# Kernel optimization log

Measured on AMD Instinct MI355X. Metric: run time of the kernel, lower is better.

Reference implementation:

```python
import jax, jax.numpy as jnp
import numpy as np

N = 50000      # nodes
E = 640000     # edges
F_IN = 128     # dataset.num_features
DIM = 128      # mParams['dim']
NC = 6         # dataset.num_classes
BN_EPS = 1e-5


def _bn_eval(z, g, b, rm, rv):
    return g * (z - rm) * jax.lax.rsqrt(rv + BN_EPS) + b


def _gin_layer(h, src, dst, W1, b1, g, be, rm, rv, W2, b2):
    # GINConv (eps=0): nn(x + sum_{j->i} x_j); messages from src aggregated at dst
    agg = jax.ops.segment_sum(h[src], dst, num_segments=N)
    z = (h + agg) @ W1 + b1
    z = jax.nn.relu(_bn_eval(z, g, be, rm, rv))
    z = jax.nn.relu(z @ W2 + b2)
    return z


def setup_inputs() -> dict:
    key = jax.random.key(0)
    ks = jax.random.split(key, 10)
    s = 1.0 / np.sqrt(DIM)
    inp = {
        'x': jax.random.normal(ks[0], (N, F_IN), jnp.float32),
        'edge_index': jax.random.randint(ks[1], (2, E), 0, N, dtype=jnp.int32),
        'batch': jnp.zeros((N,), jnp.int32),
        # conv1 MLP: Linear(F_IN,DIM) -> BN(DIM) -> ReLU -> Linear(DIM,DIM) -> ReLU
        'c1_W1': jax.random.normal(ks[2], (F_IN, DIM), jnp.float32) * s,
        'c1_b1': jnp.zeros((DIM,), jnp.float32),
        'c1_g': jnp.ones((DIM,), jnp.float32),
        'c1_beta': jnp.zeros((DIM,), jnp.float32),
        'c1_rm': jnp.zeros((DIM,), jnp.float32),
        'c1_rv': jnp.ones((DIM,), jnp.float32),
        'c1_W2': jax.random.normal(ks[3], (DIM, DIM), jnp.float32) * s,
        'c1_b2': jnp.zeros((DIM,), jnp.float32),
        # 2 extra GINConv layers (c_depth-1), stacked on leading axis
        'conv_W1': jax.random.normal(ks[4], (2, DIM, DIM), jnp.float32) * s,
        'conv_b1': jnp.zeros((2, DIM), jnp.float32),
        'conv_g': jnp.ones((2, DIM), jnp.float32),
        'conv_beta': jnp.zeros((2, DIM), jnp.float32),
        'conv_rm': jnp.zeros((2, DIM), jnp.float32),
        'conv_rv': jnp.ones((2, DIM), jnp.float32),
        'conv_W2': jax.random.normal(ks[5], (2, DIM, DIM), jnp.float32) * s,
        'conv_b2': jnp.zeros((2, DIM), jnp.float32),
        # 2 linear layers (l_depth)
        'lin_W': jax.random.normal(ks[6], (2, DIM, DIM), jnp.float32) * s,
        'lin_b': jnp.zeros((2, DIM), jnp.float32),
        # classifier Linear(2*DIM, NC)
        'cls_W': jax.random.normal(ks[7], (2 * DIM, NC), jnp.float32) * s,
        'cls_b': jnp.zeros((NC,), jnp.float32),
    }
    return inp


def reference(x, edge_index, batch,
              c1_W1, c1_b1, c1_g, c1_beta, c1_rm, c1_rv, c1_W2, c1_b2,
              conv_W1, conv_b1, conv_g, conv_beta, conv_rm, conv_rv, conv_W2, conv_b2,
              lin_W, lin_b, cls_W, cls_b):
    src, dst = edge_index[0], edge_index[1]
    h = _gin_layer(x, src, dst, c1_W1, c1_b1, c1_g, c1_beta, c1_rm, c1_rv, c1_W2, c1_b2)
    h = jax.nn.relu(h)  # extra .relu() after conv1 (idempotent)
    for i in range(conv_W1.shape[0]):
        h = _gin_layer(h, src, dst, conv_W1[i], conv_b1[i], conv_g[i], conv_beta[i],
                       conv_rm[i], conv_rv[i], conv_W2[i], conv_b2[i])
        h = jax.nn.relu(h)
    for i in range(lin_W.shape[0]):
        h = jax.nn.relu(h @ lin_W[i] + lin_b[i])
    # dropout: eval mode -> identity
    e = jnp.concatenate([h[src], h[dst]], axis=1)  # [E, 2*DIM]
    out = e @ cls_W + cls_b                         # [E, NC]
    return (out, e)
```

## Files before the change

### kernel.cpp

```cpp
#include <hip/hip_runtime.h>
#include <cstddef>
#include <cstdint>

#define NN 50000
#define EE 640000
#define FD 128

typedef float fvec4 __attribute__((ext_vector_type(4)));


__global__ __launch_bounds__(256) void k_zero(int* __restrict__ p) {
  int i = blockIdx.x * 256 + threadIdx.x;
  if (i < NN) p[i] = 0;
}

__global__ __launch_bounds__(256) void k_hist(const int* __restrict__ dst,
                                              int* __restrict__ deg) {
  int e = blockIdx.x * 256 + threadIdx.x;
  atomicAdd(&deg[dst[e]], 1);
}

__global__ __launch_bounds__(1024) void k_scan(const int* __restrict__ deg,
                                               int* __restrict__ off,
                                               int* __restrict__ cur) {
  __shared__ int wsum[16], woff[16];
  __shared__ int carryS;
  const int t = threadIdx.x, lane = t & 63, w = t >> 6;
  if (t == 0) carryS = 0;
  __syncthreads();
  for (int base = 0; base < NN; base += 4096) {
    int i = base + (t << 2);
    int4 dv = make_int4(0, 0, 0, 0);
    if (i < NN) dv = *reinterpret_cast<const int4*>(deg + i);
    int tsum = dv.x + dv.y + dv.z + dv.w;
    int incl = tsum;
#pragma unroll
    for (int d = 1; d < 64; d <<= 1) {
      int u = __shfl_up(incl, d, 64);
      if (lane >= d) incl += u;
    }
    if (lane == 63) wsum[w] = incl;
    __syncthreads();
    if (t == 0) {
      int run = 0;
#pragma unroll
      for (int k = 0; k < 16; ++k) { woff[k] = run; run += wsum[k]; }
    }
    __syncthreads();
    int ebase = (incl - tsum) + woff[w] + carryS;
    if (i < NN) {
      int4 ov;
      ov.x = ebase;
      ov.y = ebase + dv.x;
      ov.z = ov.y + dv.y;
      ov.w = ov.z + dv.z;
      *reinterpret_cast<int4*>(off + i) = ov;
      *reinterpret_cast<int4*>(cur + i) = ov;
    }
    __syncthreads();
    if (t == 0) carryS += woff[15] + wsum[15];
    __syncthreads();
  }
}

__global__ __launch_bounds__(256) void k_fill(const int* __restrict__ src,
                                              const int* __restrict__ dst,
                                              int* __restrict__ cur,
                                              int* __restrict__ ssrc) {
  int e = blockIdx.x * 256 + threadIdx.x;
  int d = dst[e];
  int pos = atomicAdd(&cur[d], 1);
  ssrc[pos] = src[e];
}

__global__ __launch_bounds__(256) void k_agg(const float* __restrict__ h,
                                             const int* __restrict__ off,
                                             const int* __restrict__ deg,
                                             const int* __restrict__ ssrc,
                                             float* __restrict__ agg) {
  int node = blockIdx.x * 8 + (threadIdx.x >> 5);
  int lane = threadIdx.x & 31;
  int f = lane << 2;
  float4 acc = *reinterpret_cast<const float4*>(h + (size_t)node * FD + f);
  int n = deg[node];
  const int* sl = ssrc + off[node];
  int j = 0;
  for (; j + 8 <= n; j += 8) {
    int s0 = sl[j], s1 = sl[j + 1], s2 = sl[j + 2], s3 = sl[j + 3];
    int s4 = sl[j + 4], s5 = sl[j + 5], s6 = sl[j + 6], s7 = sl[j + 7];
    float4 v0 = *reinterpret_cast<const float4*>(h + (size_t)s0 * FD + f);
    float4 v1 = *reinterpret_cast<const float4*>(h + (size_t)s1 * FD + f);
    float4 v2 = *reinterpret_cast<const float4*>(h + (size_t)s2 * FD + f);
    float4 v3 = *reinterpret_cast<const float4*>(h + (size_t)s3 * FD + f);
    float4 v4 = *reinterpret_cast<const float4*>(h + (size_t)s4 * FD + f);
    float4 v5 = *reinterpret_cast<const float4*>(h + (size_t)s5 * FD + f);
    float4 v6 = *reinterpret_cast<const float4*>(h + (size_t)s6 * FD + f);
    float4 v7 = *reinterpret_cast<const float4*>(h + (size_t)s7 * FD + f);
    float tx0 = (v0.x + v1.x) + (v2.x + v3.x);
    float ty0 = (v0.y + v1.y) + (v2.y + v3.y);
    float tz0 = (v0.z + v1.z) + (v2.z + v3.z);
    float tw0 = (v0.w + v1.w) + (v2.w + v3.w);
    float tx1 = (v4.x + v5.x) + (v6.x + v7.x);
    float ty1 = (v4.y + v5.y) + (v6.y + v7.y);
    float tz1 = (v4.z + v5.z) + (v6.z + v7.z);
    float tw1 = (v4.w + v5.w) + (v6.w + v7.w);
    acc.x += tx0 + tx1; acc.y += ty0 + ty1; acc.z += tz0 + tz1; acc.w += tw0 + tw1;
  }
  for (; j + 4 <= n; j += 4) {
    int s0 = sl[j], s1 = sl[j + 1], s2 = sl[j + 2], s3 = sl[j + 3];
    float4 v0 = *reinterpret_cast<const float4*>(h + (size_t)s0 * FD + f);
    float4 v1 = *reinterpret_cast<const float4*>(h + (size_t)s1 * FD + f);
    float4 v2 = *reinterpret_cast<const float4*>(h + (size_t)s2 * FD + f);
    float4 v3 = *reinterpret_cast<const float4*>(h + (size_t)s3 * FD + f);
    acc.x += (v0.x + v1.x) + (v2.x + v3.x);
    acc.y += (v0.y + v1.y) + (v2.y + v3.y);
    acc.z += (v0.z + v1.z) + (v2.z + v3.z);
    acc.w += (v0.w + v1.w) + (v2.w + v3.w);
  }
  for (; j < n; ++j) {
    int s = sl[j];
    float4 v = *reinterpret_cast<const float4*>(h + (size_t)s * FD + f);
    acc.x += v.x; acc.y += v.y; acc.z += v.z; acc.w += v.w;
  }
  *reinterpret_cast<float4*>(agg + (size_t)node * FD + f) = acc;
}

__global__ __launch_bounds__(256) void k_gemm(const float* __restrict__ A,
                                              const float* __restrict__ W,
                                              const float* __restrict__ bias,
                                              const float* __restrict__ gg,
                                              const float* __restrict__ bb,
                                              const float* __restrict__ rm,
                                              const float* __restrict__ rv,
                                              int use_bn,
                                              float* __restrict__ O, int M) {
  __shared__ float At[32][132];
  __shared__ float Ws[32][132];
  const int t  = threadIdx.x;
  const int tx = t & 15;
  const int ty = t >> 4;
  const int rowBase = blockIdx.x * 128;

  float acc[8][8] = {};

  for (int kc = 0; kc < 4; ++kc) {
    const int k0 = kc << 5;
#pragma unroll
    for (int i = 0; i < 4; ++i) {
      int fl = t + (i << 8);
      int row = fl & 127;
      int kg  = (fl >> 7) << 2;
      int r = rowBase + row;
      float4 v = make_float4(0.f, 0.f, 0.f, 0.f);
      if (r < M) v = *reinterpret_cast<const float4*>(A + (size_t)r * FD + k0 + kg);
      At[kg + 0][row] = v.x;
      At[kg + 1][row] = v.y;
      At[kg + 2][row] = v.z;
      At[kg + 3][row] = v.w;
    }
#pragma unroll
    for (int i = 0; i < 4; ++i) {
      int fl = t + (i << 8);
      int wr = fl >> 5;
      int wc = (fl & 31) << 2;
      *reinterpret_cast<float4*>(&Ws[wr][wc]) =
          *reinterpret_cast<const float4*>(W + (size_t)(k0 + wr) * FD + wc);
    }
    __syncthreads();

#pragma unroll 8
    for (int k = 0; k < 32; ++k) {
      const float4 a0 = *reinterpret_cast<const float4*>(&At[k][ty << 3]);
      const float4 a1 = *reinterpret_cast<const float4*>(&At[k][(ty << 3) + 4]);
      const float4 w0 = *reinterpret_cast<const float4*>(&Ws[k][tx << 2]);
      const float4 w1 = *reinterpret_cast<const float4*>(&Ws[k][64 + (tx << 2)]);
      const float av[8] = {a0.x, a0.y, a0.z, a0.w, a1.x, a1.y, a1.z, a1.w};
      const float wv[8] = {w0.x, w0.y, w0.z, w0.w, w1.x, w1.y, w1.z, w1.w};
#pragma unroll
      for (int i2 = 0; i2 < 8; ++i2)
#pragma unroll
        for (int j = 0; j < 8; ++j)
          acc[i2][j] = fmaf(av[i2], wv[j], acc[i2][j]);
    }
    __syncthreads();
  }

  float sc[8], sh[8];
#pragma unroll
  for (int j = 0; j < 8; ++j) {
    int c = (j < 4) ? ((tx << 2) + j) : (64 + (tx << 2) + (j - 4));
    if (use_bn) {
      float s = gg[c] * rsqrtf(rv[c] + 1e-5f);
      sc[j] = s;
      sh[j] = (bias[c] - rm[c]) * s + bb[c];
    } else {
      sc[j] = 1.f;
      sh[j] = bias[c];
    }
  }
#pragma unroll
  for (int i = 0; i < 8; ++i) {
    int r = rowBase + (ty << 3) + i;
    if (r < M) {
      float o[8];
#pragma unroll
      for (int j = 0; j < 8; ++j) {
        float v = fmaf(acc[i][j], sc[j], sh[j]);
        o[j] = v > 0.f ? v : 0.f;
      }
      *reinterpret_cast<float4*>(O + (size_t)r * FD + (tx << 2)) =
          make_float4(o[0], o[1], o[2], o[3]);
      *reinterpret_cast<float4*>(O + (size_t)r * FD + 64 + (tx << 2)) =
          make_float4(o[4], o[5], o[6], o[7]);
    }
  }
}

__global__ __launch_bounds__(256) void k_uv(const float* __restrict__ h,
                                            const float* __restrict__ clsW,
                                            float* __restrict__ U,
                                            float* __restrict__ V) {
  int node = blockIdx.x * 8 + (threadIdx.x >> 5);
  int lane = threadIdx.x & 31;
  int f = lane << 2;
  float4 v = *reinterpret_cast<const float4*>(h + (size_t)node * FD + f);
  float p[12];
#pragma unroll
  for (int c = 0; c < 6; ++c) {
    p[c] = fmaf(v.x, clsW[(size_t)(f + 0) * 6 + c],
           fmaf(v.y, clsW[(size_t)(f + 1) * 6 + c],
           fmaf(v.z, clsW[(size_t)(f + 2) * 6 + c],
                v.w * clsW[(size_t)(f + 3) * 6 + c])));
    p[6 + c] = fmaf(v.x, clsW[(size_t)(FD + f + 0) * 6 + c],
               fmaf(v.y, clsW[(size_t)(FD + f + 1) * 6 + c],
               fmaf(v.z, clsW[(size_t)(FD + f + 2) * 6 + c],
                    v.w * clsW[(size_t)(FD + f + 3) * 6 + c])));
  }
#pragma unroll
  for (int m = 16; m >= 1; m >>= 1) {
#pragma unroll
    for (int c = 0; c < 12; ++c) p[c] += __shfl_xor(p[c], m, 64);
  }
  float outv = 0.f;
#pragma unroll
  for (int c = 0; c < 12; ++c) outv = (lane == c) ? p[c] : outv;
  if (lane < 6)       U[(size_t)node * 6 + lane] = outv;
  else if (lane < 12) V[(size_t)node * 6 + (lane - 6)] = outv;
}

__global__ __launch_bounds__(256) void k_edge(const float* __restrict__ h,
                                              const int* __restrict__ src,
                                              const int* __restrict__ dst,
                                              const float* __restrict__ U,
                                              const float* __restrict__ V,
                                              const float* __restrict__ clsB,
                                              float* __restrict__ outL,
                                              float* __restrict__ outE) {
  int eid  = blockIdx.x * 4 + (threadIdx.x >> 6);
  int lane = threadIdx.x & 63;
  int s = src[eid];
  int d = dst[eid];
  int node = (lane < 32) ? s : d;
  int f = (lane & 31) << 2;
  fvec4 v = *reinterpret_cast<const fvec4*>(h + (size_t)node * FD + f);
  __builtin_nontemporal_store(v, reinterpret_cast<fvec4*>(outE + (size_t)eid * 256 + (lane << 2)));
  if (lane < 6) {
    float lv = U[(size_t)s * 6 + lane] + V[(size_t)d * 6 + lane] + clsB[lane];
    __builtin_nontemporal_store(lv, outL + (size_t)eid * 6 + lane);
  }
}

extern "C" void kernel_launch(void* const* d_in, const int* in_sizes, int n_in,
                              void* d_out, int out_size, void* d_ws, size_t ws_size,
                              hipStream_t stream) {
  const float* x     = (const float*)d_in[0];
  const int*   ei    = (const int*)d_in[1];
  const int*   src   = ei;
  const int*   dst   = ei + EE;
  const float* c1_W1 = (const float*)d_in[3];
  const float* c1_b1 = (const float*)d_in[4];
  const float* c1_g  = (const float*)d_in[5];
  const float* c1_be = (const float*)d_in[6];
  const float* c1_rm = (const float*)d_in[7];
  const float* c1_rv = (const float*)d_in[8];
  const float* c1_W2 = (const float*)d_in[9];
  const float* c1_b2 = (const float*)d_in[10];
  const float* cv_W1 = (const float*)d_in[11];
  const float* cv_b1 = (const float*)d_in[12];
  const float* cv_g  = (const float*)d_in[13];
  const float* cv_be = (const float*)d_in[14];
  const float* cv_rm = (const float*)d_in[15];
  const float* cv_rv = (const float*)d_in[16];
  const float* cv_W2 = (const float*)d_in[17];
  const float* cv_b2 = (const float*)d_in[18];
  const float* ln_W  = (const float*)d_in[19];
  const float* ln_b  = (const float*)d_in[20];
  const float* clsW  = (const float*)d_in[21];
  const float* clsB  = (const float*)d_in[22];

  float* buf0 = (float*)d_ws;
  float* buf1 = buf0 + (size_t)NN * FD;
  float* Uu   = buf1 + (size_t)NN * FD;
  float* Vv   = Uu + (size_t)NN * 6;

  float* outL = (float*)d_out;
  float* outE = outL + (size_t)EE * 6;

  const size_t outFloats = (size_t)EE * 262;
  const size_t scrInts   = (size_t)NN * 3 + (size_t)EE;
  const size_t scrStart  = (outFloats - scrInts) & ~(size_t)3;
  int* deg  = (int*)d_out + scrStart;
  int* off  = deg + NN;
  int* curp = off + NN;
  int* ssrc = curp + NN;

  dim3 B(256);
  const int gZero   = (NN + 255) / 256;
  const int gEdgeWk = EE / 256;
  const int gAgg    = NN / 8;
  const int gGemm   = (NN + 127) / 128;
  const int gUV     = NN / 8;
  const int gEdge   = EE / 4;

  k_zero<<<gZero, B, 0, stream>>>(deg);
  k_hist<<<gEdgeWk, B, 0, stream>>>(dst, deg);
  k_scan<<<1, dim3(1024), 0, stream>>>(deg, off, curp);
  k_fill<<<gEdgeWk, B, 0, stream>>>(src, dst, curp, ssrc);

  float* bufs[2] = {buf0, buf1};

  k_agg<<<gAgg, B, 0, stream>>>(x, off, deg, ssrc, buf0);
  k_gemm<<<gGemm, B, 0, stream>>>(buf0, c1_W1, c1_b1, c1_g, c1_be, c1_rm, c1_rv, 1, buf1, NN);
  k_gemm<<<gGemm, B, 0, stream>>>(buf1, c1_W2, c1_b2, nullptr, nullptr, nullptr, nullptr, 0, buf0, NN);
  int pp = 0;

  for (int l = 0; l < 2; ++l) {
    float* hc = bufs[pp];
    float* ho = bufs[1 - pp];
    k_agg<<<gAgg, B, 0, stream>>>(hc, off, deg, ssrc, ho);
    k_gemm<<<gGemm, B, 0, stream>>>(ho, cv_W1 + (size_t)l * FD * FD, cv_b1 + l * FD,
                                    cv_g + l * FD, cv_be + l * FD, cv_rm + l * FD,
                                    cv_rv + l * FD, 1, hc, NN);
    k_gemm<<<gGemm, B, 0, stream>>>(hc, cv_W2 + (size_t)l * FD * FD, cv_b2 + l * FD,
                                    nullptr, nullptr, nullptr, nullptr, 0, ho, NN);
    pp = 1 - pp;
  }

  for (int l = 0; l < 2; ++l) {
    k_gemm<<<gGemm, B, 0, stream>>>(bufs[pp], ln_W + (size_t)l * FD * FD, ln_b + l * FD,
                                    nullptr, nullptr, nullptr, nullptr, 0, bufs[1 - pp], NN);
    pp = 1 - pp;
  }

  k_uv<<<gUV, B, 0, stream>>>(bufs[pp], clsW, Uu, Vv);
  k_edge<<<gEdge, B, 0, stream>>>(bufs[pp], src, dst, Uu, Vv, clsB, outL, outE);
}
```

Baseline: 1.284 ms.

## Split neighbor aggregation across half-waves and fuse classifier into edge kernel

```diff
diff --git a/kernel.cpp b/kernel.cpp
--- a/kernel.cpp
+++ b/kernel.cpp
@@ -7,7 +7,6 @@
 #define FD 128
 
 typedef float fvec4 __attribute__((ext_vector_type(4)));
-
 
 __global__ __launch_bounds__(256) void k_zero(int* __restrict__ p) {
   int i = blockIdx.x * 256 + threadIdx.x;
@@ -78,14 +77,21 @@
                                              const int* __restrict__ deg,
                                              const int* __restrict__ ssrc,
                                              float* __restrict__ agg) {
-  int node = blockIdx.x * 8 + (threadIdx.x >> 5);
-  int lane = threadIdx.x & 31;
-  int f = lane << 2;
-  float4 acc = *reinterpret_cast<const float4*>(h + (size_t)node * FD + f);
+  int node = blockIdx.x * 4 + (threadIdx.x >> 6);
+  int lane = threadIdx.x & 63;
+  int half = lane >> 5;
+  int f = (lane & 31) << 2;
   int n = deg[node];
+  int nh = n >> 1;
   const int* sl = ssrc + off[node];
-  int j = 0;
-  for (; j + 8 <= n; j += 8) {
+
+  float4 acc = make_float4(0.f, 0.f, 0.f, 0.f);
+  if (half == 0)
+    acc = *reinterpret_cast<const float4*>(h + (size_t)node * FD + f);
+
+  int j    = half ? nh : 0;
+  int jend = half ? n  : nh;
+  for (; j + 8 <= jend; j += 8) {
     int s0 = sl[j], s1 = sl[j + 1], s2 = sl[j + 2], s3 = sl[j + 3];
     int s4 = sl[j + 4], s5 = sl[j + 5], s6 = sl[j + 6], s7 = sl[j + 7];
     float4 v0 = *reinterpret_cast<const float4*>(h + (size_t)s0 * FD + f);
@@ -96,17 +102,12 @@
     float4 v5 = *reinterpret_cast<const float4*>(h + (size_t)s5 * FD + f);
     float4 v6 = *reinterpret_cast<const float4*>(h + (size_t)s6 * FD + f);
     float4 v7 = *reinterpret_cast<const float4*>(h + (size_t)s7 * FD + f);
-    float tx0 = (v0.x + v1.x) + (v2.x + v3.x);
-    float ty0 = (v0.y + v1.y) + (v2.y + v3.y);
-    float tz0 = (v0.z + v1.z) + (v2.z + v3.z);
-    float tw0 = (v0.w + v1.w) + (v2.w + v3.w);
-    float tx1 = (v4.x + v5.x) + (v6.x + v7.x);
-    float ty1 = (v4.y + v5.y) + (v6.y + v7.y);
-    float tz1 = (v4.z + v5.z) + (v6.z + v7.z);
-    float tw1 = (v4.w + v5.w) + (v6.w + v7.w);
-    acc.x += tx0 + tx1; acc.y += ty0 + ty1; acc.z += tz0 + tz1; acc.w += tw0 + tw1;
-  }
-  for (; j + 4 <= n; j += 4) {
+    acc.x += ((v0.x + v1.x) + (v2.x + v3.x)) + ((v4.x + v5.x) + (v6.x + v7.x));
+    acc.y += ((v0.y + v1.y) + (v2.y + v3.y)) + ((v4.y + v5.y) + (v6.y + v7.y));
+    acc.z += ((v0.z + v1.z) + (v2.z + v3.z)) + ((v4.z + v5.z) + (v6.z + v7.z));
+    acc.w += ((v0.w + v1.w) + (v2.w + v3.w)) + ((v4.w + v5.w) + (v6.w + v7.w));
+  }
+  for (; j + 4 <= jend; j += 4) {
     int s0 = sl[j], s1 = sl[j + 1], s2 = sl[j + 2], s3 = sl[j + 3];
     float4 v0 = *reinterpret_cast<const float4*>(h + (size_t)s0 * FD + f);
     float4 v1 = *reinterpret_cast<const float4*>(h + (size_t)s1 * FD + f);
@@ -117,12 +118,17 @@
     acc.z += (v0.z + v1.z) + (v2.z + v3.z);
     acc.w += (v0.w + v1.w) + (v2.w + v3.w);
   }
-  for (; j < n; ++j) {
+  for (; j < jend; ++j) {
     int s = sl[j];
     float4 v = *reinterpret_cast<const float4*>(h + (size_t)s * FD + f);
     acc.x += v.x; acc.y += v.y; acc.z += v.z; acc.w += v.w;
   }
-  *reinterpret_cast<float4*>(agg + (size_t)node * FD + f) = acc;
+  acc.x += __shfl_xor(acc.x, 32, 64);
+  acc.y += __shfl_xor(acc.y, 32, 64);
+  acc.z += __shfl_xor(acc.z, 32, 64);
+  acc.w += __shfl_xor(acc.w, 32, 64);
+  if (half == 0)
+    *reinterpret_cast<float4*>(agg + (size_t)node * FD + f) = acc;
 }
 
 __global__ __launch_bounds__(256) void k_gemm(const float* __restrict__ A,
@@ -216,43 +222,10 @@
   }
 }
 
-__global__ __launch_bounds__(256) void k_uv(const float* __restrict__ h,
-                                            const float* __restrict__ clsW,
-                                            float* __restrict__ U,
-                                            float* __restrict__ V) {
-  int node = blockIdx.x * 8 + (threadIdx.x >> 5);
-  int lane = threadIdx.x & 31;
-  int f = lane << 2;
-  float4 v = *reinterpret_cast<const float4*>(h + (size_t)node * FD + f);
-  float p[12];
-#pragma unroll
-  for (int c = 0; c < 6; ++c) {
-    p[c] = fmaf(v.x, clsW[(size_t)(f + 0) * 6 + c],
-           fmaf(v.y, clsW[(size_t)(f + 1) * 6 + c],
-           fmaf(v.z, clsW[(size_t)(f + 2) * 6 + c],
-                v.w * clsW[(size_t)(f + 3) * 6 + c])));
-    p[6 + c] = fmaf(v.x, clsW[(size_t)(FD + f + 0) * 6 + c],
-               fmaf(v.y, clsW[(size_t)(FD + f + 1) * 6 + c],
-               fmaf(v.z, clsW[(size_t)(FD + f + 2) * 6 + c],
-                    v.w * clsW[(size_t)(FD + f + 3) * 6 + c])));
-  }
-#pragma unroll
-  for (int m = 16; m >= 1; m >>= 1) {
-#pragma unroll
-    for (int c = 0; c < 12; ++c) p[c] += __shfl_xor(p[c], m, 64);
-  }
-  float outv = 0.f;
-#pragma unroll
-  for (int c = 0; c < 12; ++c) outv = (lane == c) ? p[c] : outv;
-  if (lane < 6)       U[(size_t)node * 6 + lane] = outv;
-  else if (lane < 12) V[(size_t)node * 6 + (lane - 6)] = outv;
-}
-
 __global__ __launch_bounds__(256) void k_edge(const float* __restrict__ h,
                                               const int* __restrict__ src,
                                               const int* __restrict__ dst,
-                                              const float* __restrict__ U,
-                                              const float* __restrict__ V,
+                                              const float* __restrict__ clsW,
                                               const float* __restrict__ clsB,
                                               float* __restrict__ outL,
                                               float* __restrict__ outE) {
@@ -264,9 +237,23 @@
   int f = (lane & 31) << 2;
   fvec4 v = *reinterpret_cast<const fvec4*>(h + (size_t)node * FD + f);
   __builtin_nontemporal_store(v, reinterpret_cast<fvec4*>(outE + (size_t)eid * 256 + (lane << 2)));
+
+  int wb = ((lane < 32) ? 0 : FD) + f;
+  const float* w0 = clsW + (size_t)wb * 6;
+  float p[6];
+#pragma unroll
+  for (int c = 0; c < 6; ++c)
+    p[c] = fmaf(v.x, w0[c], fmaf(v.y, w0[6 + c], fmaf(v.z, w0[12 + c], v.w * w0[18 + c])));
+#pragma unroll
+  for (int m = 32; m >= 1; m >>= 1) {
+#pragma unroll
+    for (int c = 0; c < 6; ++c) p[c] += __shfl_xor(p[c], m, 64);
+  }
   if (lane < 6) {
-    float lv = U[(size_t)s * 6 + lane] + V[(size_t)d * 6 + lane] + clsB[lane];
-    __builtin_nontemporal_store(lv, outL + (size_t)eid * 6 + lane);
+    float outv = 0.f;
+#pragma unroll
+    for (int c = 0; c < 6; ++c) outv = (lane == c) ? p[c] : outv;
+    __builtin_nontemporal_store(outv + clsB[lane], outL + (size_t)eid * 6 + lane);
   }
 }
 
@@ -300,8 +287,6 @@
 
   float* buf0 = (float*)d_ws;
   float* buf1 = buf0 + (size_t)NN * FD;
-  float* Uu   = buf1 + (size_t)NN * FD;
-  float* Vv   = Uu + (size_t)NN * 6;
 
   float* outL = (float*)d_out;
   float* outE = outL + (size_t)EE * 6;
@@ -317,9 +302,8 @@
   dim3 B(256);
   const int gZero   = (NN + 255) / 256;
   const int gEdgeWk = EE / 256;
-  const int gAgg    = NN / 8;
+  const int gAgg    = NN / 4;
   const int gGemm   = (NN + 127) / 128;
-  const int gUV     = NN / 8;
   const int gEdge   = EE / 4;
 
   k_zero<<<gZero, B, 0, stream>>>(deg);
@@ -352,6 +336,5 @@
     pp = 1 - pp;
   }
 
-  k_uv<<<gUV, B, 0, stream>>>(bufs[pp], clsW, Uu, Vv);
-  k_edge<<<gEdge, B, 0, stream>>>(bufs[pp], src, dst, Uu, Vv, clsB, outL, outE);
-}
+  k_edge<<<gEdge, B, 0, stream>>>(bufs[pp], src, dst, clsW, clsB, outL, outE);
+}
```

Result: no change. 1.309 ms (+1.9%).
